# Kernel tuning notes

Hardware: AMD Instinct MI355X
Metric: run time of the kernel (lower is better)

Reference implementation:

```python
import jax, jax.numpy as jnp
import numpy as np

B, C, D, NL = 2, 32, 96, 4
H1, RH, RE, NR = 64, 256, 128, 100
EPS = 1e-5

def setup_inputs() -> dict:
    key = jax.random.key(0)
    ks = jax.random.split(key, 14)
    V = D * D * D
    return {
        'data': jax.random.normal(ks[0], (B, 1, D, D, D), jnp.float32),
        'atlas_mask': jax.random.uniform(ks[1], (NR, V), jnp.float32),
        'conv0_w': jax.random.normal(ks[2], (C, 1, 3, 3, 3), jnp.float32) * 0.1,
        'conv0_b': jax.random.normal(ks[3], (C,), jnp.float32) * 0.01,
        'convk_w': jax.random.normal(ks[4], (NL - 1, C, C, 3, 3, 3), jnp.float32) * 0.05,
        'convk_b': jax.random.normal(ks[5], (NL - 1, C), jnp.float32) * 0.01,
        'sw1': jax.random.normal(ks[6], (NR, C, H1), jnp.float32) * 0.1,
        'sb1': jax.random.normal(ks[7], (NR, H1), jnp.float32) * 0.01,
        'sw2': jax.random.normal(ks[8], (NR, H1, C), jnp.float32) * 0.1,
        'sb2': jax.random.normal(ks[9], (NR, C), jnp.float32) * 0.01,
        'pw1': jax.random.normal(ks[10], (NR, C, RH), jnp.float32) * 0.1,
        'pb1': jax.random.normal(ks[11], (NR, RH), jnp.float32) * 0.01,
        'pw2': jax.random.normal(ks[12], (NR, RH, RE), jnp.float32) * 0.05,
        'pb2': jax.random.normal(ks[13], (NR, RE), jnp.float32) * 0.01,
    }

def _inorm(x):
    # InstanceNorm3d, affine=False: normalize over spatial dims per (n, c)
    m = x.mean(axis=(2, 3, 4), keepdims=True)
    v = x.var(axis=(2, 3, 4), keepdims=True)
    return (x - m) * jax.lax.rsqrt(v + EPS)

def _conv_block(x, w, b):
    y = jax.lax.conv_general_dilated(
        x, w, window_strides=(1, 1, 1), padding='SAME',
        dimension_numbers=('NCDHW', 'OIDHW', 'NCDHW'))
    return jax.nn.relu(_inorm(y + b[None, :, None, None, None]))

def reference(data, atlas_mask, conv0_w, conv0_b, convk_w, convk_b,
              sw1, sb1, sw2, sb2, pw1, pb1, pw2, pb2):
    emb = _conv_block(data, conv0_w, conv0_b)
    for i in range(NL - 1):
        emb = _conv_block(emb, convk_w[i], convk_b[i])
    flat = emb.reshape(B, C, -1)                      # [B, C, V]
    # atlas masked pooling: [B,C,V] @ [V,NR] -> [B,NR,C], mean over mask
    roi = jnp.einsum('bcv,rv->brc', flat, atlas_mask)
    roi = roi / atlas_mask.sum(axis=-1)[None, :, None]
    # per-ROI scale MLP (batched expert GEMMs) + sigmoid gate
    h = jax.nn.relu(jnp.einsum('brc,rch->brh', roi, sw1) + sb1[None])
    scale = jax.nn.sigmoid(jnp.einsum('brh,rhc->brc', h, sw2) + sb2[None])
    sf = scale * roi
    # per-ROI projection MLP
    h2 = jax.nn.relu(jnp.einsum('brc,rch->brh', sf, pw1) + pb1[None])
    out = jnp.einsum('brh,rhe->bre', h2, pw2) + pb2[None]
    return out  # [B, NR, RE]
```

## Files before the change

kernel.cpp:

```cpp
#include <hip/hip_runtime.h>
#include <stdint.h>

#define DD 96
#define VV (96*96*96)
#define EPSN 1e-5f

typedef short short8 __attribute__((ext_vector_type(8)));
typedef float floatx4 __attribute__((ext_vector_type(4)));

__device__ __forceinline__ float bf2f(uint32_t u_lo16) {
    union { uint32_t i; float f; } x; x.i = u_lo16 << 16; return x.f;
}
__device__ __forceinline__ uint16_t f2bf(float f) {
    union { float f; uint32_t i; } x; x.f = f;
    uint32_t r = x.i + 0x7FFFu + ((x.i >> 16) & 1u);
    return (uint16_t)(r >> 16);
}
__device__ __forceinline__ uint32_t cvtpk(float lo, float hi) {
    uint32_t r;
    asm("v_cvt_pk_bf16_f32 %0, %1, %2" : "=v"(r) : "v"(lo), "v"(hi));
    return r;
}

__global__ void k_packw(const float* __restrict__ w0, const float* __restrict__ wk,
                        float* __restrict__ wT0, uint16_t* __restrict__ wpk) {
    int i = blockIdx.x * 256 + threadIdx.x;
    if (i < 27 * 32) {
        int co = i / 27, k = i % 27;
        wT0[k * 32 + co] = w0[i];
    }
    int j = i - 27 * 32;
    if (j >= 0 && j < 3 * 27 * 2 * 512) {
        int e = j & 7, l = (j >> 3) & 63, nt = (j >> 9) & 1;
        int r = j >> 10;
        int tap = r % 27, li = r / 27;
        int co = nt * 16 + (l & 15), ci = (l >> 4) * 8 + e;
        float v = wk[((li * 32 + co) * 32 + ci) * 27 + tap];
        wpk[j] = f2bf(v);
    }
}

__global__ __launch_bounds__(192) void k_conv0(const float* __restrict__ data,
        const float* __restrict__ wT0, uint16_t* __restrict__ out,
        float2* __restrict__ spart) {
    const int y = blockIdx.x, z = blockIdx.y, b = blockIdx.z;
    const int t = threadIdx.x, co = t & 31, xs = t >> 5;
    const int xb4 = 16 * xs - 4;
    __shared__ float ws[27 * 32];
    __shared__ float wpart[3][32][2];
    for (int i = t; i < 27 * 32; i += 192) ws[i] = wT0[i];
    __syncthreads();

    float acc[16];
#pragma unroll
    for (int j = 0; j < 16; ++j) acc[j] = 0.f;

#pragma unroll 3
    for (int row = 0; row < 9; ++row) {
        int dz = row / 3 - 1, dy = row % 3 - 1;
        int vz = z + dz, vy = y + dy;
        bool rowok = (vz >= 0 && vz < DD && vy >= 0 && vy < DD);
        const float* rp = data + (long long)b * VV + (long long)(vz * 96 + vy) * 96;
        float v[24];
#pragma unroll
        for (int k = 0; k < 6; ++k) {
            int start = xb4 + 4 * k;
            float4 f = make_float4(0.f, 0.f, 0.f, 0.f);
            if (rowok && start >= 0 && start <= 92) f = *(const float4*)(rp + start);
            v[4 * k] = f.x; v[4 * k + 1] = f.y; v[4 * k + 2] = f.z; v[4 * k + 3] = f.w;
        }
        float w0 = ws[(row * 3 + 0) * 32 + co];
        float w1 = ws[(row * 3 + 1) * 32 + co];
        float w2 = ws[(row * 3 + 2) * 32 + co];
#pragma unroll
        for (int j = 0; j < 16; ++j)
            acc[j] = fmaf(v[j + 3], w0, fmaf(v[j + 4], w1, fmaf(v[j + 5], w2, acc[j])));
    }
    float s1 = 0.f, s2 = 0.f;
#pragma unroll
    for (int j = 0; j < 16; ++j) { s1 += acc[j]; s2 += acc[j] * acc[j]; }
    s1 += __shfl_xor(s1, 32, 64);
    s2 += __shfl_xor(s2, 32, 64);
    int wv = t >> 6;
    if ((t & 63) < 32) { wpart[wv][co][0] = s1; wpart[wv][co][1] = s2; }
    __syncthreads();
    if (t < 32) {
        float a = 0.f, c2 = 0.f;
#pragma unroll
        for (int w = 0; w < 3; ++w) { a += wpart[w][t][0]; c2 += wpart[w][t][1]; }
        int zone = z * 96 + y;
        spart[(zone * 2 + b) * 32 + t] = make_float2(a, c2);
    }
    long long obase = ((long long)b * VV + (long long)(z * 96 + y) * 96 + 16 * xs) * 32 + co;
#pragma unroll
    for (int j = 0; j < 16; ++j)
        out[obase + (long long)j * 32] = f2bf(acc[j]);
}

__global__ void k_finalize(const float2* __restrict__ spart, float2* __restrict__ mr) {
    const int bc = blockIdx.x, t = threadIdx.x;
    float a = 0.f, s2 = 0.f;
    for (int z = t; z < 9216; z += 256) {
        float2 v = spart[z * 64 + bc];
        a += v.x; s2 += v.y;
    }
#pragma unroll
    for (int m = 1; m < 64; m <<= 1) {
        a  += __shfl_xor(a, m, 64);
        s2 += __shfl_xor(s2, m, 64);
    }
    __shared__ float2 wred[4];
    if ((t & 63) == 0) wred[t >> 6] = make_float2(a, s2);
    __syncthreads();
    if (t == 0) {
        float A = wred[0].x + wred[1].x + wred[2].x + wred[3].x;
        float S = wred[0].y + wred[1].y + wred[2].y + wred[3].y;
        float mean = A / (float)VV;
        float var = S / (float)VV - mean * mean;
        float rs = rsqrtf(fmaxf(var, 0.f) + EPSN);
        mr[bc] = make_float2(mean, rs);
    }
}

template<int CHFIRST>
__global__ __launch_bounds__(512, 4) void k_convk_v3(const uint16_t* __restrict__ in,
        const float2* __restrict__ mrprev, const uint16_t* __restrict__ wpk,
        uint16_t* __restrict__ out, float2* __restrict__ spart) {
    __shared__ uint16_t a_s[10 * 3136];

    int bid = (int)blockIdx.x;
    bid = (bid & 7) * 288 + (bid >> 3);
    const int yg = bid % 12; int tmp = bid / 12;
    const int z = tmp % 96; const int b = tmp / 96;
    const int t = threadIdx.x;
    const int w = t >> 6, lane = t & 63;
    const int y = yg * 8 + w;
    const int vx = lane & 15, kg = lane >> 4;

    const int cig = t & 3, vgrp = t >> 2;
    float nAr[8], nBr[8];
#pragma unroll
    for (int e = 0; e < 8; ++e) {
        float2 v = mrprev[b * 32 + cig * 8 + e];
        nAr[e] = v.y;
        nBr[e] = -v.x * v.y;
    }

    if (t < 160) {
        int row = t >> 4, half = (t >> 3) & 1, o8 = t & 7;
        *((uint2*)&a_s[row * 3136 + (half ? 97 * 32 : 0) + o8 * 4]) = make_uint2(0, 0);
    }

    floatx4 acc[6][2];
#pragma unroll
    for (int mt = 0; mt < 6; ++mt) {
        acc[mt][0] = (floatx4){0.f, 0.f, 0.f, 0.f};
        acc[mt][1] = (floatx4){0.f, 0.f, 0.f, 0.f};
    }

    const uint16_t* inb = in + (long long)b * VV * 32;

    for (int dz = 0; dz < 3; ++dz) {
        const int zp = z + dz - 1;
        const bool zok = (unsigned)zp < 96u;
        __syncthreads();
#pragma unroll
        for (int j = 0; j < 8; ++j) {
            int v = vgrp + j * 128;
            if (v < 960) {
                int row = v / 96;
                int x = v - row * 96;
                int yp = yg * 8 + row - 1;
                uint4 o4 = make_uint4(0, 0, 0, 0);
                if (zok && (unsigned)yp < 96u) {
                    uint4 raw = *(const uint4*)(inb +
                        (((long long)zp * 96 + yp) * 96 + x) * 32 + cig * 8);
                    uint32_t u[4] = {raw.x, raw.y, raw.z, raw.w};
#pragma unroll
                    for (int e = 0; e < 4; ++e) {
                        float lo = bf2f(u[e] & 0xFFFFu);
                        union { uint32_t i; float f; } hv; hv.i = u[e] & 0xFFFF0000u;
                        float x0 = fmaxf(0.f, fmaf(lo,   nAr[2 * e],     nBr[2 * e]));
                        float x1 = fmaxf(0.f, fmaf(hv.f, nAr[2 * e + 1], nBr[2 * e + 1]));
                        o4.x = e == 0 ? cvtpk(x0, x1) : o4.x;
                        o4.y = e == 1 ? cvtpk(x0, x1) : o4.y;
                        o4.z = e == 2 ? cvtpk(x0, x1) : o4.z;
                        o4.w = e == 3 ? cvtpk(x0, x1) : o4.w;
                    }
                }
                *((uint4*)&a_s[row * 3136 + (x + 1) * 32 + cig * 8]) = o4;
            }
        }
        __syncthreads();
        const uint16_t* wpt = wpk + dz * 9216;
#pragma unroll
        for (int dy = 0; dy < 3; ++dy) {
            const uint16_t* as_row = &a_s[(w + dy) * 3136];
#pragma unroll
            for (int dx = 0; dx < 3; ++dx) {
                const int tl = dy * 3 + dx;
                const short8 wb0 = *(const short8*)&wpt[(tl * 2 + 0) * 512 + lane * 8];
                const short8 wb1 = *(const short8*)&wpt[(tl * 2 + 1) * 512 + lane * 8];
#pragma unroll
                for (int mt = 0; mt < 6; ++mt) {
                    const short8 a = *(const short8*)&as_row[(mt * 16 + vx + dx) * 32 + kg * 8];
                    acc[mt][0] = __builtin_amdgcn_mfma_f32_16x16x32_bf16(a, wb0, acc[mt][0], 0, 0, 0);
                    acc[mt][1] = __builtin_amdgcn_mfma_f32_16x16x32_bf16(a, wb1, acc[mt][1], 0, 0, 0);
                }
            }
        }
    }

    float s1n0 = 0.f, s2n0 = 0.f, s1n1 = 0.f, s2n1 = 0.f;
#pragma unroll
    for (int mt = 0; mt < 6; ++mt)
#pragma unroll
        for (int j = 0; j < 4; ++j) {
            float v0 = acc[mt][0][j], v1 = acc[mt][1][j];
            s1n0 += v0; s2n0 += v0 * v0;
            s1n1 += v1; s2n1 += v1 * v1;
        }
    s1n0 += __shfl_xor(s1n0, 16, 64); s1n0 += __shfl_xor(s1n0, 32, 64);
    s2n0 += __shfl_xor(s2n0, 16, 64); s2n0 += __shfl_xor(s2n0, 32, 64);
    s1n1 += __shfl_xor(s1n1, 16, 64); s1n1 += __shfl_xor(s1n1, 32, 64);
    s2n1 += __shfl_xor(s2n1, 16, 64); s2n1 += __shfl_xor(s2n1, 32, 64);
    if (lane < 16) {
        int zone = z * 96 + y;
        spart[(zone * 2 + b) * 32 + lane]      = make_float2(s1n0, s2n0);
        spart[(zone * 2 + b) * 32 + lane + 16] = make_float2(s1n1, s2n1);
    }

    if (CHFIRST) {
        long long vbase = (long long)(z * 96 + y) * 96;
#pragma unroll
        for (int mt = 0; mt < 6; ++mt)
#pragma unroll
            for (int nt = 0; nt < 2; ++nt) {
                uint32_t lo = (uint32_t)f2bf(acc[mt][nt][0]) | ((uint32_t)f2bf(acc[mt][nt][1]) << 16);
                uint32_t hi = (uint32_t)f2bf(acc[mt][nt][2]) | ((uint32_t)f2bf(acc[mt][nt][3]) << 16);
                long long co = b * 32 + nt * 16 + vx;
                uint2* dst = (uint2*)&out[co * VV + vbase + mt * 16 + kg * 4];
                *dst = make_uint2(lo, hi);
            }
    } else {
        long long obase = ((long long)b * VV + (long long)(z * 96 + y) * 96) * 32;
#pragma unroll
        for (int mt = 0; mt < 6; ++mt)
#pragma unroll
            for (int nt = 0; nt < 2; ++nt)
#pragma unroll
                for (int j = 0; j < 4; ++j)
                    out[obase + (long long)(mt * 16 + kg * 4 + j) * 32 + nt * 16 + vx] =
                        f2bf(acc[mt][nt][j]);
    }
}

__global__ __launch_bounds__(448) void k_pool_mfma(const uint16_t* __restrict__ emb,
        const float* __restrict__ mask, const float2* __restrict__ mr,
        float* __restrict__ rzone, float* __restrict__ mzone) {
    const int t = threadIdx.x;
    const int rt = t >> 6, lane = t & 63;
    const int rl = lane & 15, kq = lane >> 4;
    const int r = rt * 16 + rl;
    const int rc = min(r, 99);
    const long long v0 = (long long)blockIdx.x * 2048;

    float nA[4], nB[4];
#pragma unroll
    for (int bct = 0; bct < 4; ++bct) {
        float2 v = mr[bct * 16 + rl];
        nA[bct] = v.y;
        nB[bct] = -v.x * v.y;
    }

    floatx4 acc[4];
#pragma unroll
    for (int bct = 0; bct < 4; ++bct) acc[bct] = (floatx4){0.f, 0.f, 0.f, 0.f};
    float msum = 0.f;

    const float* mrow = mask + (long long)rc * VV + v0 + kq * 8;
    const uint16_t* eb0 = emb + (long long)(0 * 16 + rl) * VV + v0 + kq * 8;
    const uint16_t* eb1 = emb + (long long)(1 * 16 + rl) * VV + v0 + kq * 8;
    const uint16_t* eb2 = emb + (long long)(2 * 16 + rl) * VV + v0 + kq * 8;
    const uint16_t* eb3 = emb + (long long)(3 * 16 + rl) * VV + v0 + kq * 8;
    const uint16_t* ebase[4] = {eb0, eb1, eb2, eb3};

#pragma unroll 2
    for (int ks = 0; ks < 64; ++ks) {
        const float4 a0 = *(const float4*)(mrow + ks * 32);
        const float4 a1 = *(const float4*)(mrow + ks * 32 + 4);
        msum += (a0.x + a0.y + a0.z + a0.w) + (a1.x + a1.y + a1.z + a1.w);
        union { uint32_t u[4]; short8 s; } af;
        af.u[0] = cvtpk(a0.x, a0.y);
        af.u[1] = cvtpk(a0.z, a0.w);
        af.u[2] = cvtpk(a1.x, a1.y);
        af.u[3] = cvtpk(a1.z, a1.w);
#pragma unroll
        for (int bct = 0; bct < 4; ++bct) {
            uint4 raw = *(const uint4*)(ebase[bct] + ks * 32);
            uint32_t u[4] = {raw.x, raw.y, raw.z, raw.w};
            union { uint32_t u[4]; short8 s; } bfr;
#pragma unroll
            for (int e = 0; e < 4; ++e) {
                float lo = bf2f(u[e] & 0xFFFFu);
                union { uint32_t i; float f; } hv; hv.i = u[e] & 0xFFFF0000u;
                float x0 = fmaxf(0.f, fmaf(lo,   nA[bct], nB[bct]));
                float x1 = fmaxf(0.f, fmaf(hv.f, nA[bct], nB[bct]));
                bfr.u[e] = cvtpk(x0, x1);
            }
            acc[bct] = __builtin_amdgcn_mfma_f32_16x16x32_bf16(af.s, bfr.s, acc[bct], 0, 0, 0);
        }
    }

    msum += __shfl_xor(msum, 16, 64);
    msum += __shfl_xor(msum, 32, 64);
    if (lane < 16 && r < 100)
        mzone[blockIdx.x * 100 + r] = msum;

#pragma unroll
    for (int bct = 0; bct < 4; ++bct)
#pragma unroll
        for (int reg = 0; reg < 4; ++reg) {
            int rr = rt * 16 + kq * 4 + reg;
            if (rr < 100)
                rzone[((long long)blockIdx.x * 100 + rr) * 64 + bct * 16 + rl] = acc[bct][reg];
        }
}

__global__ void k_roifin(const float* __restrict__ rzone, const float* __restrict__ mzone,
                         float* __restrict__ roi) {
    const int r = blockIdx.x, t = threadIdx.x;
    __shared__ float sred[256];
    float ms = 0.f;
    for (int z = t; z < 432; z += 256) ms += mzone[z * 100 + r];
    sred[t] = ms;
    __syncthreads();
    for (int s = 128; s > 0; s >>= 1) {
        if (t < s) sred[t] += sred[t + s];
        __syncthreads();
    }
    float msum = sred[0];
    const int bc = t & 63, zs = t >> 6;
    float a = 0.f;
    for (int z = zs; z < 432; z += 4) a += rzone[((long long)z * 100 + r) * 64 + bc];
    __shared__ float s2[4][64];
    s2[zs][bc] = a;
    __syncthreads();
    if (t < 64) {
        float v = s2[0][t] + s2[1][t] + s2[2][t] + s2[3][t];
        int b = t >> 5, c = t & 31;
        roi[(b * 100 + r) * 32 + c] = v / msum;
    }
}

__global__ __launch_bounds__(256) void k_mlp(const float* __restrict__ roi,
        const float* __restrict__ sw1, const float* __restrict__ sb1,
        const float* __restrict__ sw2, const float* __restrict__ sb2,
        const float* __restrict__ pw1, const float* __restrict__ pb1,
        const float* __restrict__ pw2, const float* __restrict__ pb2,
        float* __restrict__ outp) {
    const int r = blockIdx.x, b = blockIdx.y, t = threadIdx.x;
    __shared__ float roi_s[32], h1_s[64], sf_s[32], h2_s[256], part[128];
    if (t < 32) roi_s[t] = roi[(b * 100 + r) * 32 + t];
    __syncthreads();
    if (t < 64) {
        float a = sb1[r * 64 + t];
        for (int c = 0; c < 32; ++c) a += roi_s[c] * sw1[(r * 32 + c) * 64 + t];
        h1_s[t] = fmaxf(a, 0.f);
    }
    __syncthreads();
    if (t < 32) {
        float a = sb2[r * 32 + t];
        for (int h = 0; h < 64; ++h) a += h1_s[h] * sw2[(r * 64 + h) * 32 + t];
        float sg = 1.f / (1.f + expf(-a));
        sf_s[t] = sg * roi_s[t];
    }
    __syncthreads();
    {
        float a = pb1[r * 256 + t];
        for (int c = 0; c < 32; ++c) a += sf_s[c] * pw1[(r * 32 + c) * 256 + t];
        h2_s[t] = fmaxf(a, 0.f);
    }
    __syncthreads();
    {
        const int e = t & 127, hh = t >> 7;
        float a = 0.f;
        for (int h = hh * 128; h < hh * 128 + 128; ++h)
            a += h2_s[h] * pw2[(r * 256 + h) * 128 + e];
        if (hh) part[e] = a;
        __syncthreads();
        if (t < 128) outp[(b * 100 + r) * 128 + t] = part[t] + a + pb2[r * 128 + t];
    }
}

extern "C" void kernel_launch(void* const* d_in, const int* in_sizes, int n_in,
                              void* d_out, int out_size, void* d_ws, size_t ws_size,
                              hipStream_t stream) {
    const float* data = (const float*)d_in[0];
    const float* mask = (const float*)d_in[1];
    const float* w0   = (const float*)d_in[2];
    const float* wk   = (const float*)d_in[4];
    const float* sw1  = (const float*)d_in[6];
    const float* sb1  = (const float*)d_in[7];
    const float* sw2  = (const float*)d_in[8];
    const float* sb2  = (const float*)d_in[9];
    const float* pw1  = (const float*)d_in[10];
    const float* pb1  = (const float*)d_in[11];
    const float* pw2  = (const float*)d_in[12];
    const float* pb2  = (const float*)d_in[13];
    float* out = (float*)d_out;

    char* ws = (char*)d_ws;
    size_t off = 0;
    auto alloc = [&](size_t bytes) {
        void* p = ws + off;
        off += (bytes + 255) & ~(size_t)255;
        return p;
    };
    uint16_t* buf0 = (uint16_t*)alloc((size_t)2 * VV * 32 * 2);
    uint16_t* buf1 = (uint16_t*)alloc((size_t)2 * VV * 32 * 2);
    float* wT0     = (float*)alloc(27 * 32 * 4);
    uint16_t* wpk  = (uint16_t*)alloc((size_t)3 * 27 * 2 * 512 * 2);
    float2* spart  = (float2*)alloc((size_t)9216 * 2 * 32 * 8);
    float2* mr     = (float2*)alloc(4 * 64 * 8);
    float* rzone   = (float*)alloc((size_t)432 * 100 * 64 * 4);
    float* mzone   = (float*)alloc((size_t)432 * 100 * 4);
    float* roi     = (float*)alloc(2 * 100 * 32 * 4);
    (void)ws_size; (void)in_sizes; (void)n_in; (void)out_size;

    k_packw<<<328, 256, 0, stream>>>(w0, wk, wT0, wpk);

    dim3 cgrid(96, 96, 2);
    k_conv0<<<cgrid, 192, 0, stream>>>(data, wT0, buf0, spart);
    k_finalize<<<64, 256, 0, stream>>>((const float2*)spart, mr + 0);

    k_convk_v3<0><<<2304, 512, 0, stream>>>(buf0, mr + 0,   wpk + 0 * 27648, buf1, spart);
    k_finalize<<<64, 256, 0, stream>>>((const float2*)spart, mr + 64);

    k_convk_v3<0><<<2304, 512, 0, stream>>>(buf1, mr + 64,  wpk + 1 * 27648, buf0, spart);
    k_finalize<<<64, 256, 0, stream>>>((const float2*)spart, mr + 128);

    k_convk_v3<1><<<2304, 512, 0, stream>>>(buf0, mr + 128, wpk + 2 * 27648, buf1, spart);
    k_finalize<<<64, 256, 0, stream>>>((const float2*)spart, mr + 192);

    k_pool_mfma<<<432, 448, 0, stream>>>(buf1, mask, mr + 192, rzone, mzone);
    k_roifin<<<100, 256, 0, stream>>>(rzone, mzone, roi);

    k_mlp<<<dim3(100, 2), 256, 0, stream>>>(roi, sw1, sb1, sw2, sb2,
                                            pw1, pb1, pw2, pb2, out);
}
```

Baseline: 919.8 us.

## Shrink conv tiles to four rows and prefetch next z-slab into registers

The 3x3x3 conv kernel now processes 4 output rows per 256-thread block instead of 8 rows per 512-thread block. This roughly halves LDS per block, and part of the next dz input slab is prefetched into registers while the current slab is written to shared memory, so global load latency overlaps the staging work. The pooling kernel is split into twice as many blocks over half-size voxel chunks to add parallelism, and the ROI finalize reduction now sums 864 partials. The smaller tiles raise the halo-reload ratio (6 input rows per 4 output rows versus 10 per 8), and the extra prefetch registers may reduce occupancy.

Result: slower. 1.545 ms (+68.0%).

```diff
diff --git a/kernel.cpp b/kernel.cpp
--- a/kernel.cpp
+++ b/kernel.cpp
@@ -123,18 +123,18 @@
 }
 
 template<int CHFIRST>
-__global__ __launch_bounds__(512, 4) void k_convk_v3(const uint16_t* __restrict__ in,
+__global__ __launch_bounds__(256, 4) void k_convk_v4(const uint16_t* __restrict__ in,
         const float2* __restrict__ mrprev, const uint16_t* __restrict__ wpk,
         uint16_t* __restrict__ out, float2* __restrict__ spart) {
-    __shared__ uint16_t a_s[10 * 3136];
+    __shared__ uint16_t a_s[6 * 3136];
 
     int bid = (int)blockIdx.x;
-    bid = (bid & 7) * 288 + (bid >> 3);
-    const int yg = bid % 12; int tmp = bid / 12;
+    bid = (bid & 7) * 576 + (bid >> 3);
+    const int yg = bid % 24; int tmp = bid / 24;
     const int z = tmp % 96; const int b = tmp / 96;
     const int t = threadIdx.x;
     const int w = t >> 6, lane = t & 63;
-    const int y = yg * 8 + w;
+    const int y = yg * 4 + w;
     const int vx = lane & 15, kg = lane >> 4;
 
     const int cig = t & 3, vgrp = t >> 2;
@@ -146,9 +146,9 @@
         nBr[e] = -v.x * v.y;
     }
 
-    if (t < 160) {
-        int row = t >> 4, half = (t >> 3) & 1, o8 = t & 7;
-        *((uint2*)&a_s[row * 3136 + (half ? 97 * 32 : 0) + o8 * 4]) = make_uint2(0, 0);
+    if (t < 48) {
+        int row = t >> 3, rem = t & 7, end = rem >> 2, q = rem & 3;
+        *((uint4*)&a_s[row * 3136 + (end ? 97 * 32 : 0) + q * 8]) = make_uint4(0, 0, 0, 0);
     }
 
     floatx4 acc[6][2];
@@ -159,37 +159,81 @@
     }
 
     const uint16_t* inb = in + (long long)b * VV * 32;
+
+    uint4 u4[5];
+    {
+        int zp = z - 1;
+        bool zok = zp >= 0;
+#pragma unroll
+        for (int j = 0; j < 5; ++j) {
+            int v = vgrp + j * 64;
+            int row = v / 96, x = v - row * 96;
+            int yp = yg * 4 + row - 1;
+            u4[j] = make_uint4(0, 0, 0, 0);
+            if (zok && (unsigned)yp < 96u)
+                u4[j] = *(const uint4*)(inb + (((long long)zp * 96 + yp) * 96 + x) * 32 + cig * 8);
+        }
+    }
 
     for (int dz = 0; dz < 3; ++dz) {
         const int zp = z + dz - 1;
         const bool zok = (unsigned)zp < 96u;
         __syncthreads();
 #pragma unroll
-        for (int j = 0; j < 8; ++j) {
-            int v = vgrp + j * 128;
-            if (v < 960) {
-                int row = v / 96;
-                int x = v - row * 96;
-                int yp = yg * 8 + row - 1;
-                uint4 o4 = make_uint4(0, 0, 0, 0);
-                if (zok && (unsigned)yp < 96u) {
-                    uint4 raw = *(const uint4*)(inb +
-                        (((long long)zp * 96 + yp) * 96 + x) * 32 + cig * 8);
-                    uint32_t u[4] = {raw.x, raw.y, raw.z, raw.w};
-#pragma unroll
-                    for (int e = 0; e < 4; ++e) {
-                        float lo = bf2f(u[e] & 0xFFFFu);
-                        union { uint32_t i; float f; } hv; hv.i = u[e] & 0xFFFF0000u;
-                        float x0 = fmaxf(0.f, fmaf(lo,   nAr[2 * e],     nBr[2 * e]));
-                        float x1 = fmaxf(0.f, fmaf(hv.f, nAr[2 * e + 1], nBr[2 * e + 1]));
-                        o4.x = e == 0 ? cvtpk(x0, x1) : o4.x;
-                        o4.y = e == 1 ? cvtpk(x0, x1) : o4.y;
-                        o4.z = e == 2 ? cvtpk(x0, x1) : o4.z;
-                        o4.w = e == 3 ? cvtpk(x0, x1) : o4.w;
-                    }
+        for (int j = 0; j < 5; ++j) {
+            int v = vgrp + j * 64;
+            int row = v / 96, x = v - row * 96;
+            int yp = yg * 4 + row - 1;
+            uint4 o4 = make_uint4(0, 0, 0, 0);
+            if (zok && (unsigned)yp < 96u) {
+                uint32_t u[4] = {u4[j].x, u4[j].y, u4[j].z, u4[j].w};
+                uint32_t o[4];
+#pragma unroll
+                for (int e = 0; e < 4; ++e) {
+                    float lo = bf2f(u[e] & 0xFFFFu);
+                    union { uint32_t i; float f; } hv; hv.i = u[e] & 0xFFFF0000u;
+                    float x0 = fmaxf(0.f, fmaf(lo,   nAr[2 * e],     nBr[2 * e]));
+                    float x1 = fmaxf(0.f, fmaf(hv.f, nAr[2 * e + 1], nBr[2 * e + 1]));
+                    o[e] = cvtpk(x0, x1);
                 }
-                *((uint4*)&a_s[row * 3136 + (x + 1) * 32 + cig * 8]) = o4;
-            }
+                o4 = make_uint4(o[0], o[1], o[2], o[3]);
+            }
+            *((uint4*)&a_s[row * 3136 + (x + 1) * 32 + cig * 8]) = o4;
+        }
+        if (dz < 2) {
+            int zp2 = z + dz;
+            bool zok2 = zp2 < 96;
+#pragma unroll
+            for (int j = 0; j < 5; ++j) {
+                int v = vgrp + j * 64;
+                int row = v / 96, x = v - row * 96;
+                int yp = yg * 4 + row - 1;
+                u4[j] = make_uint4(0, 0, 0, 0);
+                if (zok2 && (unsigned)yp < 96u)
+                    u4[j] = *(const uint4*)(inb + (((long long)zp2 * 96 + yp) * 96 + x) * 32 + cig * 8);
+            }
+        }
+#pragma unroll
+        for (int j = 5; j < 9; ++j) {
+            int v = vgrp + j * 64;
+            int row = v / 96, x = v - row * 96;
+            int yp = yg * 4 + row - 1;
+            uint4 o4 = make_uint4(0, 0, 0, 0);
+            if (zok && (unsigned)yp < 96u) {
+                uint4 raw = *(const uint4*)(inb + (((long long)zp * 96 + yp) * 96 + x) * 32 + cig * 8);
+                uint32_t u[4] = {raw.x, raw.y, raw.z, raw.w};
+                uint32_t o[4];
+#pragma unroll
+                for (int e = 0; e < 4; ++e) {
+                    float lo = bf2f(u[e] & 0xFFFFu);
+                    union { uint32_t i; float f; } hv; hv.i = u[e] & 0xFFFF0000u;
+                    float x0 = fmaxf(0.f, fmaf(lo,   nAr[2 * e],     nBr[2 * e]));
+                    float x1 = fmaxf(0.f, fmaf(hv.f, nAr[2 * e + 1], nBr[2 * e + 1]));
+                    o[e] = cvtpk(x0, x1);
+                }
+                o4 = make_uint4(o[0], o[1], o[2], o[3]);
+            }
+            *((uint4*)&a_s[row * 3136 + (x + 1) * 32 + cig * 8]) = o4;
         }
         __syncthreads();
         const uint16_t* wpt = wpk + dz * 9216;
@@ -263,7 +307,7 @@
     const int rl = lane & 15, kq = lane >> 4;
     const int r = rt * 16 + rl;
     const int rc = min(r, 99);
-    const long long v0 = (long long)blockIdx.x * 2048;
+    const long long v0 = (long long)blockIdx.x * 1024;
 
     float nA[4], nB[4];
 #pragma unroll
@@ -286,7 +330,7 @@
     const uint16_t* ebase[4] = {eb0, eb1, eb2, eb3};
 
 #pragma unroll 2
-    for (int ks = 0; ks < 64; ++ks) {
+    for (int ks = 0; ks < 32; ++ks) {
         const float4 a0 = *(const float4*)(mrow + ks * 32);
         const float4 a1 = *(const float4*)(mrow + ks * 32 + 4);
         msum += (a0.x + a0.y + a0.z + a0.w) + (a1.x + a1.y + a1.z + a1.w);
@@ -332,7 +376,7 @@
     const int r = blockIdx.x, t = threadIdx.x;
     __shared__ float sred[256];
     float ms = 0.f;
-    for (int z = t; z < 432; z += 256) ms += mzone[z * 100 + r];
+    for (int z = t; z < 864; z += 256) ms += mzone[z * 100 + r];
     sred[t] = ms;
     __syncthreads();
     for (int s = 128; s > 0; s >>= 1) {
@@ -342,7 +386,7 @@
     float msum = sred[0];
     const int bc = t & 63, zs = t >> 6;
     float a = 0.f;
-    for (int z = zs; z < 432; z += 4) a += rzone[((long long)z * 100 + r) * 64 + bc];
+    for (int z = zs; z < 864; z += 4) a += rzone[((long long)z * 100 + r) * 64 + bc];
     __shared__ float s2[4][64];
     s2[zs][bc] = a;
     __syncthreads();
@@ -423,8 +467,8 @@
     uint16_t* wpk  = (uint16_t*)alloc((size_t)3 * 27 * 2 * 512 * 2);
     float2* spart  = (float2*)alloc((size_t)9216 * 2 * 32 * 8);
     float2* mr     = (float2*)alloc(4 * 64 * 8);
-    float* rzone   = (float*)alloc((size_t)432 * 100 * 64 * 4);
-    float* mzone   = (float*)alloc((size_t)432 * 100 * 4);
+    float* rzone   = (float*)alloc((size_t)864 * 100 * 64 * 4);
+    float* mzone   = (float*)alloc((size_t)864 * 100 * 4);
     float* roi     = (float*)alloc(2 * 100 * 32 * 4);
     (void)ws_size; (void)in_sizes; (void)n_in; (void)out_size;
 
@@ -434,16 +478,16 @@
     k_conv0<<<cgrid, 192, 0, stream>>>(data, wT0, buf0, spart);
     k_finalize<<<64, 256, 0, stream>>>((const float2*)spart, mr + 0);
 
-    k_convk_v3<0><<<2304, 512, 0, stream>>>(buf0, mr + 0,   wpk + 0 * 27648, buf1, spart);
+    k_convk_v4<0><<<4608, 256, 0, stream>>>(buf0, mr + 0,   wpk + 0 * 27648, buf1, spart);
     k_finalize<<<64, 256, 0, stream>>>((const float2*)spart, mr + 64);
 
-    k_convk_v3<0><<<2304, 512, 0, stream>>>(buf1, mr + 64,  wpk + 1 * 27648, buf0, spart);
+    k_convk_v4<0><<<4608, 256, 0, stream>>>(buf1, mr + 64,  wpk + 1 * 27648, buf0, spart);
     k_finalize<<<64, 256, 0, stream>>>((const float2*)spart, mr + 128);
 
-    k_convk_v3<1><<<2304, 512, 0, stream>>>(buf0, mr + 128, wpk + 2 * 27648, buf1, spart);
+    k_convk_v4<1><<<4608, 256, 0, stream>>>(buf0, mr + 128, wpk + 2 * 27648, buf1, spart);
     k_finalize<<<64, 256, 0, stream>>>((const float2*)spart, mr + 192);
 
-    k_pool_mfma<<<432, 448, 0, stream>>>(buf1, mask, mr + 192, rzone, mzone);
+    k_pool_mfma<<<864, 448, 0, stream>>>(buf1, mask, mr + 192, rzone, mzone);
     k_roifin<<<100, 256, 0, stream>>>(rzone, mzone, roi);
 
     k_mlp<<<dim3(100, 2), 256, 0, stream>>>(roi, sw1, sb1, sw2, sb2,
```
